# Kernel tuning notes

Measured on AMD Instinct MI355X. Metric: run time of the kernel, lower is better.

The kernel has to match this reference:

```python
import jax, jax.numpy as jnp
import numpy as np

H = 32            # hidden_size
BURN = 256        # burn_in_offset
TRUNC = 1024      # train_truncate


def setup_inputs() -> dict:
    key = jax.random.key(0)
    ks = jax.random.split(key, 9)
    B, T = 64, 256 + 47 * 1024  # 48384
    s = 1.0 / np.sqrt(H)        # PyTorch LSTM init scale
    x = jax.random.normal(ks[0], (B, T, 1), dtype=jnp.float32)
    h0 = jnp.zeros((1, H), jnp.float32)
    c0 = jnp.zeros((1, H), jnp.float32)
    W_ih = jax.random.uniform(ks[1], (4 * H, 1), jnp.float32, -s, s)
    W_hh = jax.random.uniform(ks[2], (4 * H, H), jnp.float32, -s, s)
    b_ih = jax.random.uniform(ks[3], (4 * H,), jnp.float32, -s, s)
    b_hh = jax.random.uniform(ks[4], (4 * H,), jnp.float32, -s, s)
    # _LSTM.reset_parameters tweak: input-gate bias -2, forget-gate bias +2
    tweak = jnp.concatenate([jnp.full((H,), -2.0), jnp.full((H,), 2.0), jnp.zeros((2 * H,))])
    b_ih = b_ih + tweak
    b_hh = b_hh + tweak
    W_head = jax.random.uniform(ks[5], (1, H), jnp.float32, -s, s)
    b_head = jax.random.uniform(ks[6], (1,), jnp.float32, -s, s)
    return {"x": x, "h0": h0, "c0": c0, "W_ih": W_ih, "W_hh": W_hh,
            "b_ih": b_ih, "b_hh": b_hh, "W_head": W_head, "b_head": b_head}


def _lstm_features(x, h0, c0, W_ih, W_hh, b_ih, b_hh):
    """Training-path LSTM: burn-in chunk (outputs detached) + TBPTT chunks."""
    B, T, _ = x.shape
    # gates order in PyTorch: i, f, g, o. Precompute input projection once.
    xp = jnp.einsum('btk,gk->btg', x, W_ih) + b_ih + b_hh   # [B, T, 4H]

    def cell(carry, xg):            # xg: [B, 4H]
        h, c = carry
        g = xg + h @ W_hh.T
        i, f, gg, o = jnp.split(g, 4, axis=-1)
        c = jax.nn.sigmoid(f) * c + jax.nn.sigmoid(i) * jnp.tanh(gg)
        h = jax.nn.sigmoid(o) * jnp.tanh(c)
        return (h, c), h

    carry = (jnp.broadcast_to(h0, (B, H)), jnp.broadcast_to(c0, (B, H)))
    # burn-in: outputs detached, hidden state carried forward un-detached
    carry, ys_burn = jax.lax.scan(cell, carry, xp[:, :BURN].transpose(1, 0, 2))
    ys_burn = jax.lax.stop_gradient(ys_burn)            # [BURN, B, H]

    n_chunks = (T - BURN) // TRUNC
    # [n_chunks, TRUNC, B, 4H]
    xp_rest = xp[:, BURN:].reshape(B, n_chunks, TRUNC, 4 * H).transpose(1, 2, 0, 3)

    def chunk_body(carry, xc):
        new_carry, ys = jax.lax.scan(cell, carry, xc)
        # detach hidden state between truncation chunks (TBPTT)
        return jax.tree_util.tree_map(jax.lax.stop_gradient, new_carry), ys

    _, ys_chunks = jax.lax.scan(chunk_body, carry, xp_rest)  # [n_chunks, TRUNC, B, H]
    ys = jnp.concatenate([ys_burn, ys_chunks.reshape(n_chunks * TRUNC, B, H)], axis=0)
    return ys.transpose(1, 0, 2)                         # [B, T, H]


def reference(x, h0, c0, W_ih, W_hh, b_ih, b_hh, W_head, b_head):
    feats = _lstm_features(x, h0, c0, W_ih, W_hh, b_ih, b_hh)
    return feats @ W_head.T + b_head                     # [B, T, 1]
```

## Files before the change

kernel.cpp:

```cpp
#include <hip/hip_runtime.h>

#define HDIM 32

typedef float v2f __attribute__((ext_vector_type(2)));
typedef unsigned int v2u __attribute__((ext_vector_type(2)));

#define KEEPF(v) asm("" : "+v"(v))

__device__ inline float fast_exp2(float x) {
#if __has_builtin(__builtin_amdgcn_exp2f)
  return __builtin_amdgcn_exp2f(x);
#else
  return exp2f(x);
#endif
}
__device__ inline float fast_rcp(float x) {
#if __has_builtin(__builtin_amdgcn_rcpf)
  return __builtin_amdgcn_rcpf(x);
#else
  return 1.0f / x;
#endif
}

__device__ inline float xchg32_for_high(float a) {
#if __has_builtin(__builtin_amdgcn_permlane32_swap)
  v2u r = __builtin_amdgcn_permlane32_swap(
      __float_as_uint(a), __float_as_uint(a), false, false);
  return __uint_as_float(r.x);
#else
  return __shfl_xor(a, 32);
#endif
}
__device__ inline float sum_halves(float p) {
#if __has_builtin(__builtin_amdgcn_permlane32_swap)
  v2u r = __builtin_amdgcn_permlane32_swap(
      __float_as_uint(p), __float_as_uint(p), false, false);
  return __uint_as_float(r.x) + __uint_as_float(r.y);
#else
  return p + __shfl_xor(p, 32);
#endif
}

__device__ inline float bcast_hi(float v, int m) {
  return __int_as_float(__builtin_amdgcn_readlane(__float_as_int(v), 32 + m));
}

__global__ __launch_bounds__(64)
__attribute__((amdgpu_waves_per_eu(1, 1)))
void lstm_fused(
    const float* __restrict__ x,
    const float* __restrict__ h0,
    const float* __restrict__ c0,
    const float* __restrict__ W_ih,
    const float* __restrict__ W_hh,
    const float* __restrict__ b_ih,
    const float* __restrict__ b_hh,
    const float* __restrict__ W_head,
    const float* __restrict__ b_head,
    float* __restrict__ y,
    int T)
{
  const int lane = threadIdx.x;
  const int b    = blockIdx.x;
  const int k    = lane & 31;
  const int j1   = lane;
  const int j2   = lane + 64;

  v2f W12[HDIM];
#pragma unroll
  for (int q = 0; q < HDIM / 4; ++q) {
    const float4 va = *reinterpret_cast<const float4*>(W_hh + j1 * HDIM + q * 4);
    const float4 vb = *reinterpret_cast<const float4*>(W_hh + j2 * HDIM + q * 4);
    W12[q * 4 + 0][0] = va.x; W12[q * 4 + 1][0] = va.y;
    W12[q * 4 + 2][0] = va.z; W12[q * 4 + 3][0] = va.w;
    W12[q * 4 + 0][1] = vb.x; W12[q * 4 + 1][1] = vb.y;
    W12[q * 4 + 2][1] = vb.z; W12[q * 4 + 3][1] = vb.w;
  }
#pragma unroll
  for (int m = 0; m < HDIM; ++m) { KEEPF(W12[m][0]); KEEPF(W12[m][1]); }

  v2f wih;  wih[0]  = W_ih[j1];            wih[1]  = W_ih[j2];
  v2f bias; bias[0] = b_ih[j1] + b_hh[j1]; bias[1] = b_ih[j2] + b_hh[j2];
  KEEPF(wih[0]); KEEPF(wih[1]); KEEPF(bias[0]); KEEPF(bias[1]);
  float wh = W_head[k];
  float bh = b_head[0];
  KEEPF(wh); KEEPF(bh);

  const bool  low  = lane < HDIM;
  const float LOG2E = 1.4426950408889634f;
  float m2L = low ? (-2.0f * LOG2E) : (-LOG2E);
  float sA  = low ? 2.0f : 1.0f;
  float bA  = low ? -1.0f : 0.0f;
  KEEPF(m2L); KEEPF(sA); KEEPF(bA);

  float h = h0[k];
  float c = c0[k];

  const float* xb = x + (size_t)b * T;
  float*       yb = y + (size_t)b * T;

  __shared__ float hb[32][68];

#pragma unroll 1
  for (int t0 = 0; t0 < T; t0 += 32) {
    float xs[32];
#pragma unroll
    for (int q = 0; q < 8; ++q) {
      float4 v = *reinterpret_cast<const float4*>(xb + t0 + q * 4);
      KEEPF(v.x); KEEPF(v.y); KEEPF(v.z); KEEPF(v.w);
      xs[q * 4 + 0] = v.x; xs[q * 4 + 1] = v.y;
      xs[q * 4 + 2] = v.z; xs[q * 4 + 3] = v.w;
    }

#pragma unroll
    for (int tt = 0; tt < 32; ++tt) {
      const float xt = xs[tt];
      v2f a0; a0[0] = fmaf(xt, wih[0], bias[0]); a0[1] = fmaf(xt, wih[1], bias[1]);
      v2f a1; a1[0] = 0.f; a1[1] = 0.f;
      v2f a2; a2[0] = 0.f; a2[1] = 0.f;
      v2f a3; a3[0] = 0.f; a3[1] = 0.f;
#pragma unroll
      for (int m = 0; m < HDIM; m += 4) {
        const float h0b = bcast_hi(h, m + 0);
        const float h1b = bcast_hi(h, m + 1);
        const float h2b = bcast_hi(h, m + 2);
        const float h3b = bcast_hi(h, m + 3);
        v2f t;
        t[0] = h0b; t[1] = h0b; a0 = __builtin_elementwise_fma(t, W12[m + 0], a0);
        t[0] = h1b; t[1] = h1b; a1 = __builtin_elementwise_fma(t, W12[m + 1], a1);
        t[0] = h2b; t[1] = h2b; a2 = __builtin_elementwise_fma(t, W12[m + 2], a2);
        t[0] = h3b; t[1] = h3b; a3 = __builtin_elementwise_fma(t, W12[m + 3], a3);
      }
      const v2f g = (a0 + a1) + (a2 + a3);

      const float e1 = fast_exp2(g[0] * (-LOG2E));
      const float p1 = fast_rcp(1.0f + e1);
      const float e2 = fast_exp2(g[1] * m2L);
      const float s2 = fast_rcp(1.0f + e2);
      const float p2 = fmaf(s2, sA, bA);

      const float a  = p1 * p2;
      const float e  = xchg32_for_high(a);

      c = fmaf(p1, c, e);
      const float ec = fast_exp2(c * (-2.0f * LOG2E));
      const float tc = fmaf(fast_rcp(1.0f + ec), 2.0f, -1.0f);
      h = p2 * tc;

      hb[tt][lane] = h * wh;
    }

    {
      const int r = k;
      const float* row = &hb[r][32 + ((lane >> 5) << 4)];
      const float4 s0 = *reinterpret_cast<const float4*>(row + 0);
      const float4 s1 = *reinterpret_cast<const float4*>(row + 4);
      const float4 s2 = *reinterpret_cast<const float4*>(row + 8);
      const float4 s3 = *reinterpret_cast<const float4*>(row + 12);
      const float p = ((s0.x + s0.y) + (s0.z + s0.w))
                    + ((s1.x + s1.y) + (s1.z + s1.w))
                    + ((s2.x + s2.y) + (s2.z + s2.w))
                    + ((s3.x + s3.y) + (s3.z + s3.w));
      const float tot = sum_halves(p) + bh;
      if (lane < 32) yb[t0 + r] = tot;
    }
  }
}

extern "C" void kernel_launch(void* const* d_in, const int* in_sizes, int n_in,
                              void* d_out, int out_size, void* d_ws, size_t ws_size,
                              hipStream_t stream) {
  const float* x      = (const float*)d_in[0];
  const float* h0     = (const float*)d_in[1];
  const float* c0     = (const float*)d_in[2];
  const float* W_ih   = (const float*)d_in[3];
  const float* W_hh   = (const float*)d_in[4];
  const float* b_ih   = (const float*)d_in[5];
  const float* b_hh   = (const float*)d_in[6];
  const float* W_head = (const float*)d_in[7];
  const float* b_head = (const float*)d_in[8];
  float* yout = (float*)d_out;

  const int B = 64;
  const int T = in_sizes[0] / B;

  lstm_fused<<<dim3(B), dim3(64), 0, stream>>>(
      x, h0, c0, W_ih, W_hh, b_ih, b_hh, W_head, b_head, yout, T);
}
```

Baseline: 9.784 ms.

## Split recurrent matvec across wave halves using ds_bpermute and permlane32 swap

```diff
diff --git a/kernel.cpp b/kernel.cpp
--- a/kernel.cpp
+++ b/kernel.cpp
@@ -31,6 +31,15 @@
   return __shfl_xor(a, 32);
 #endif
 }
+__device__ inline float from_counterpart(float v, bool low) {
+#if __has_builtin(__builtin_amdgcn_permlane32_swap)
+  v2u r = __builtin_amdgcn_permlane32_swap(
+      __float_as_uint(v), __float_as_uint(v), false, false);
+  return low ? __uint_as_float(r.y) : __uint_as_float(r.x);
+#else
+  return __shfl_xor(v, 32);
+#endif
+}
 __device__ inline float sum_halves(float p) {
 #if __has_builtin(__builtin_amdgcn_permlane32_swap)
   v2u r = __builtin_amdgcn_permlane32_swap(
@@ -39,10 +48,6 @@
 #else
   return p + __shfl_xor(p, 32);
 #endif
-}
-
-__device__ inline float bcast_hi(float v, int m) {
-  return __int_as_float(__builtin_amdgcn_readlane(__float_as_int(v), 32 + m));
 }
 
 __global__ __launch_bounds__(64)
@@ -63,21 +68,33 @@
   const int lane = threadIdx.x;
   const int b    = blockIdx.x;
   const int k    = lane & 31;
+  const int half = lane >> 5;
+  const int m0   = half << 4;
   const int j1   = lane;
   const int j2   = lane + 64;
-
-  v2f W12[HDIM];
-#pragma unroll
-  for (int q = 0; q < HDIM / 4; ++q) {
-    const float4 va = *reinterpret_cast<const float4*>(W_hh + j1 * HDIM + q * 4);
-    const float4 vb = *reinterpret_cast<const float4*>(W_hh + j2 * HDIM + q * 4);
-    W12[q * 4 + 0][0] = va.x; W12[q * 4 + 1][0] = va.y;
-    W12[q * 4 + 2][0] = va.z; W12[q * 4 + 3][0] = va.w;
-    W12[q * 4 + 0][1] = vb.x; W12[q * 4 + 1][1] = vb.y;
-    W12[q * 4 + 2][1] = vb.z; W12[q * 4 + 3][1] = vb.w;
+  const int j1o  = lane ^ 32;
+  const int j2o  = (lane ^ 32) + 64;
+  const bool low = (half == 0);
+
+  const int bpbase = 128 + (half << 6);
+
+  v2f Wself[16], Wothr[16];
+#pragma unroll
+  for (int q = 0; q < 4; ++q) {
+    const float4 va = *reinterpret_cast<const float4*>(W_hh + j1  * HDIM + m0 + q * 4);
+    const float4 vb = *reinterpret_cast<const float4*>(W_hh + j2  * HDIM + m0 + q * 4);
+    const float4 vc = *reinterpret_cast<const float4*>(W_hh + j1o * HDIM + m0 + q * 4);
+    const float4 vd = *reinterpret_cast<const float4*>(W_hh + j2o * HDIM + m0 + q * 4);
+    Wself[q*4+0][0] = va.x; Wself[q*4+1][0] = va.y; Wself[q*4+2][0] = va.z; Wself[q*4+3][0] = va.w;
+    Wself[q*4+0][1] = vb.x; Wself[q*4+1][1] = vb.y; Wself[q*4+2][1] = vb.z; Wself[q*4+3][1] = vb.w;
+    Wothr[q*4+0][0] = vc.x; Wothr[q*4+1][0] = vc.y; Wothr[q*4+2][0] = vc.z; Wothr[q*4+3][0] = vc.w;
+    Wothr[q*4+0][1] = vd.x; Wothr[q*4+1][1] = vd.y; Wothr[q*4+2][1] = vd.z; Wothr[q*4+3][1] = vd.w;
   }
 #pragma unroll
-  for (int m = 0; m < HDIM; ++m) { KEEPF(W12[m][0]); KEEPF(W12[m][1]); }
+  for (int s = 0; s < 16; ++s) {
+    KEEPF(Wself[s][0]); KEEPF(Wself[s][1]);
+    KEEPF(Wothr[s][0]); KEEPF(Wothr[s][1]);
+  }
 
   v2f wih;  wih[0]  = W_ih[j1];            wih[1]  = W_ih[j2];
   v2f bias; bias[0] = b_ih[j1] + b_hh[j1]; bias[1] = b_ih[j2] + b_hh[j2];
@@ -86,7 +103,6 @@
   float bh = b_head[0];
   KEEPF(wh); KEEPF(bh);
 
-  const bool  low  = lane < HDIM;
   const float LOG2E = 1.4426950408889634f;
   float m2L = low ? (-2.0f * LOG2E) : (-LOG2E);
   float sA  = low ? 2.0f : 1.0f;
@@ -115,23 +131,31 @@
 #pragma unroll
     for (int tt = 0; tt < 32; ++tt) {
       const float xt = xs[tt];
-      v2f a0; a0[0] = fmaf(xt, wih[0], bias[0]); a0[1] = fmaf(xt, wih[1], bias[1]);
-      v2f a1; a1[0] = 0.f; a1[1] = 0.f;
-      v2f a2; a2[0] = 0.f; a2[1] = 0.f;
-      v2f a3; a3[0] = 0.f; a3[1] = 0.f;
-#pragma unroll
-      for (int m = 0; m < HDIM; m += 4) {
-        const float h0b = bcast_hi(h, m + 0);
-        const float h1b = bcast_hi(h, m + 1);
-        const float h2b = bcast_hi(h, m + 2);
-        const float h3b = bcast_hi(h, m + 3);
-        v2f t;
-        t[0] = h0b; t[1] = h0b; a0 = __builtin_elementwise_fma(t, W12[m + 0], a0);
-        t[0] = h1b; t[1] = h1b; a1 = __builtin_elementwise_fma(t, W12[m + 1], a1);
-        t[0] = h2b; t[1] = h2b; a2 = __builtin_elementwise_fma(t, W12[m + 2], a2);
-        t[0] = h3b; t[1] = h3b; a3 = __builtin_elementwise_fma(t, W12[m + 3], a3);
+
+      const int hbits = __float_as_int(h);
+      float B[16];
+#pragma unroll
+      for (int s = 0; s < 16; ++s)
+        B[s] = __int_as_float(__builtin_amdgcn_ds_bpermute(bpbase + 4 * s, hbits));
+
+      v2f aS0; aS0[0] = fmaf(xt, wih[0], bias[0]); aS0[1] = fmaf(xt, wih[1], bias[1]);
+      v2f aS1; aS1[0] = 0.f; aS1[1] = 0.f;
+      v2f aO0; aO0[0] = 0.f; aO0[1] = 0.f;
+      v2f aO1; aO1[0] = 0.f; aO1[1] = 0.f;
+#pragma unroll
+      for (int s = 0; s < 16; s += 2) {
+        v2f t0v; t0v[0] = B[s];     t0v[1] = B[s];
+        v2f t1v; t1v[0] = B[s + 1]; t1v[1] = B[s + 1];
+        aS0 = __builtin_elementwise_fma(t0v, Wself[s],     aS0);
+        aS1 = __builtin_elementwise_fma(t1v, Wself[s + 1], aS1);
+        aO0 = __builtin_elementwise_fma(t0v, Wothr[s],     aO0);
+        aO1 = __builtin_elementwise_fma(t1v, Wothr[s + 1], aO1);
       }
-      const v2f g = (a0 + a1) + (a2 + a3);
+      const v2f aS = aS0 + aS1;
+      const v2f aO = aO0 + aO1;
+      v2f g;
+      g[0] = aS[0] + from_counterpart(aO[0], low);
+      g[1] = aS[1] + from_counterpart(aO[1], low);
 
       const float e1 = fast_exp2(g[0] * (-LOG2E));
       const float p1 = fast_rcp(1.0f + e1);
@@ -152,7 +176,7 @@
 
     {
       const int r = k;
-      const float* row = &hb[r][32 + ((lane >> 5) << 4)];
+      const float* row = &hb[r][32 + (half << 4)];
       const float4 s0 = *reinterpret_cast<const float4*>(row + 0);
       const float4 s1 = *reinterpret_cast<const float4*>(row + 4);
       const float4 s2 = *reinterpret_cast<const float4*>(row + 8);
```

Measured after the change: 11.75 ms. +20.1%, slower.
